# Optimization experiments

Hardware: AMD Instinct MI355X
Metric: run time of the kernel (lower is better)

The kernel has to match this reference:

```python
import jax, jax.numpy as jnp
import numpy as np

N_NODES = 131072
N_EDGES = 262144
N_GRAPHS = 4096
EMB = 300
N_LAYER = 5
N_TASKS = 1
NUM_ATOM_TYPE = 120
NUM_CHIRALITY = 3
NUM_BOND_TYPE = 6   # includes self-loop type 4
NUM_BOND_DIR = 3
SELF_LOOP_TYPE = 4
BN_EPS = 1e-5


def setup_inputs() -> dict:
    key = jax.random.key(0)
    ks = jax.random.split(key, 20)
    x = jnp.stack([
        jax.random.randint(ks[0], (N_NODES,), 0, NUM_ATOM_TYPE, dtype=jnp.int32),
        jax.random.randint(ks[1], (N_NODES,), 0, NUM_CHIRALITY, dtype=jnp.int32),
    ], axis=1)
    edge_index = jax.random.randint(ks[2], (2, N_EDGES), 0, N_NODES, dtype=jnp.int32)
    edge_attr = jnp.stack([
        jax.random.randint(ks[3], (N_EDGES,), 0, 4, dtype=jnp.int32),
        jax.random.randint(ks[4], (N_EDGES,), 0, NUM_BOND_DIR, dtype=jnp.int32),
    ], axis=1)
    # sorted batch vector, every graph non-empty (32 nodes per graph)
    batch = jnp.repeat(jnp.arange(N_GRAPHS, dtype=jnp.int32), N_NODES // N_GRAPHS)
    s = 0.05
    params = {
        'atom_emb0': jax.random.normal(ks[5], (NUM_ATOM_TYPE, EMB), jnp.float32) * s,
        'atom_emb1': jax.random.normal(ks[6], (NUM_CHIRALITY, EMB), jnp.float32) * s,
        'bond_emb0': jax.random.normal(ks[7], (N_LAYER, NUM_BOND_TYPE, EMB), jnp.float32) * s,
        'bond_emb1': jax.random.normal(ks[8], (N_LAYER, NUM_BOND_DIR, EMB), jnp.float32) * s,
        'W1': jax.random.normal(ks[9], (N_LAYER, EMB, 2 * EMB), jnp.float32) * s,
        'b1': jnp.zeros((N_LAYER, 2 * EMB), jnp.float32),
        'W2': jax.random.normal(ks[10], (N_LAYER, 2 * EMB, EMB), jnp.float32) * s,
        'b2': jnp.zeros((N_LAYER, EMB), jnp.float32),
        'bn_gamma': jnp.ones((N_LAYER, EMB), jnp.float32),
        'bn_beta': jnp.zeros((N_LAYER, EMB), jnp.float32),
        'head_W1': jax.random.normal(ks[11], (EMB, EMB // 2), jnp.float32) * s,
        'head_b1': jnp.zeros((EMB // 2,), jnp.float32),
        'head_W2': jax.random.normal(ks[12], (EMB // 2, N_TASKS), jnp.float32) * s,
        'head_b2': jnp.zeros((N_TASKS,), jnp.float32),
    }
    return dict(x=x, edge_index=edge_index, edge_attr=edge_attr, batch=batch,
                num_graphs=N_GRAPHS, **params)


def _gnn_forward(x, edge_index, edge_attr, batch, num_graphs,
                 atom_emb0, atom_emb1, bond_emb0, bond_emb1,
                 W1, b1, W2, b2, bn_gamma, bn_beta,
                 head_W1, head_b1, head_W2, head_b2):
    n = x.shape[0]
    L = W1.shape[0]
    # add self loops with bond type SELF_LOOP_TYPE
    loop = jnp.arange(n, dtype=edge_index.dtype)
    src = jnp.concatenate([edge_index[0], loop])
    dst = jnp.concatenate([edge_index[1], loop])
    ea0 = jnp.concatenate([edge_attr[:, 0], jnp.full((n,), SELF_LOOP_TYPE, edge_attr.dtype)])
    ea1 = jnp.concatenate([edge_attr[:, 1], jnp.zeros((n,), edge_attr.dtype)])

    h = atom_emb0[x[:, 0]] + atom_emb1[x[:, 1]]  # [N, EMB]
    for l in range(L):
        e = bond_emb0[l][ea0] + bond_emb1[l][ea1]           # [E+N, EMB]
        msg = h[src] + e                                     # gather + add
        agg = jax.ops.segment_sum(msg, dst, num_segments=n)  # [N, EMB]
        hid = jax.nn.relu(agg @ W1[l] + b1[l])
        h2 = hid @ W2[l] + b2[l]
        # BatchNorm1d (training-mode batch stats)
        mean = jnp.mean(h2, axis=0)
        var = jnp.var(h2, axis=0)
        h2 = (h2 - mean) * jax.lax.rsqrt(var + BN_EPS) * bn_gamma[l] + bn_beta[l]
        h = h2 if l == L - 1 else jax.nn.relu(h2)
    # super_node_rep: last node of each graph (batch is sorted)
    last_idx = jax.ops.segment_max(jnp.arange(n), batch, num_segments=num_graphs)
    sup = h[last_idx]                                        # [G, EMB]
    out = jax.nn.elu(sup @ head_W1 + head_b1) @ head_W2 + head_b2
    return out                                               # [G, num_tasks]


def reference(x, edge_index, edge_attr, batch, num_graphs,
              atom_emb0, atom_emb1, bond_emb0, bond_emb1,
              W1, b1, W2, b2, bn_gamma, bn_beta,
              head_W1, head_b1, head_W2, head_b2):
    return _gnn_forward(x, edge_index, edge_attr, batch, num_graphs,
                        atom_emb0, atom_emb1, bond_emb0, bond_emb1,
                        W1, b1, W2, b2, bn_gamma, bn_beta,
                        head_W1, head_b1, head_W2, head_b2)
```

## Files before the change

kernel.cpp:

```cpp
#include <hip/hip_runtime.h>
#include <hip/hip_bf16.h>

#define NN 131072
#define NE 262144
#define NG 4096
#define EMB 300
#define HS 320
#define K1 320
#define N1 640
#define N2P 384
#define NLAYER 5
#define NRB (NN / 128)

typedef __attribute__((ext_vector_type(8))) short short8;
typedef __attribute__((ext_vector_type(4))) float f32x4;
typedef __attribute__((ext_vector_type(4))) unsigned short ushort4v;

__device__ __forceinline__ void gload_lds16(const void* g, void* l) {
  __builtin_amdgcn_global_load_lds((const __attribute__((address_space(1))) void*)g,
                                   (__attribute__((address_space(3))) void*)l, 16, 0, 0);
}
__device__ __forceinline__ float b2f(unsigned short u) {
  return __uint_as_float(((unsigned)u) << 16);
}
__device__ __forceinline__ unsigned short f2b(float x) {
  __hip_bfloat16 b = __float2bfloat16(x);
  return *(unsigned short*)&b;
}


__global__ void prep_w1(const float* __restrict__ W1, __hip_bfloat16* __restrict__ W1T) {
  int idx = blockIdx.x * 256 + threadIdx.x;
  if (idx >= NLAYER * N1 * K1) return;
  int l = idx / (N1 * K1); int r = idx % (N1 * K1);
  int n = r / K1; int k = r % K1;
  float v = (n < 600 && k < 300) ? W1[(size_t)(l * 300 + k) * 600 + n] : 0.f;
  W1T[idx] = __float2bfloat16(v);
}

__global__ void prep_w2(const float* __restrict__ W2, __hip_bfloat16* __restrict__ W2T) {
  int idx = blockIdx.x * 256 + threadIdx.x;
  if (idx >= NLAYER * N2P * N1) return;
  int l = idx / (N2P * N1); int r = idx % (N2P * N1);
  int n = r / N1; int k = r % N1;
  float v = (n < 300 && k < 600) ? W2[(size_t)(l * 600 + k) * 300 + n] : 0.f;
  W2T[idx] = __float2bfloat16(v);
}

__global__ void prep_bias(const float* __restrict__ b1, const float* __restrict__ b2,
                          float* __restrict__ b1p, float* __restrict__ b2p) {
  int idx = blockIdx.x * 256 + threadIdx.x;
  if (idx < NLAYER * N1) {
    int l = idx / N1, n = idx % N1;
    b1p[idx] = (n < 600) ? b1[l * 600 + n] : 0.f;
  } else {
    int k = idx - NLAYER * N1;
    if (k < NLAYER * N2P) {
      int l = k / N2P, n = k % N2P;
      b2p[k] = (n < 300) ? b2[l * 300 + n] : 0.f;
    }
  }
}

__global__ void init_h(const int* __restrict__ x, const float* __restrict__ ae0,
                       const float* __restrict__ ae1, __hip_bfloat16* __restrict__ h) {
  int v = blockIdx.x; int t = threadIdx.x;
  int x0 = x[2 * v], x1 = x[2 * v + 1];
  for (int c = t; c < HS; c += 256)
    h[(size_t)v * HS + c] = __float2bfloat16(c < EMB ? ae0[x0 * EMB + c] + ae1[x1 * EMB + c] : 0.f);
}


__global__ void count_edges(const int* __restrict__ ei, int* __restrict__ counts) {
  int j = blockIdx.x * 256 + threadIdx.x;
  if (j >= NE) return;
  atomicAdd(&counts[ei[NE + j]], 1);
}

__global__ void scan_block(const int* __restrict__ counts, int* __restrict__ indptr,
                           int* __restrict__ blockSums) {
  __shared__ int s[256];
  int b = blockIdx.x, t = threadIdx.x;
  int base = b * 1024 + t * 4;
  int4 c = *(const int4*)&counts[base];
  int tsum = c.x + c.y + c.z + c.w;
  s[t] = tsum;
  __syncthreads();
  for (int off = 1; off < 256; off <<= 1) {
    int v = (t >= off) ? s[t - off] : 0;
    __syncthreads();
    s[t] += v;
    __syncthreads();
  }
  int excl = (t == 0) ? 0 : s[t - 1];
  indptr[base + 0] = excl;
  indptr[base + 1] = excl + c.x;
  indptr[base + 2] = excl + c.x + c.y;
  indptr[base + 3] = excl + c.x + c.y + c.z;
  if (t == 255) blockSums[b] = s[255];
}

__global__ void scan_top(const int* __restrict__ blockSums, int* __restrict__ blockOff) {
  __shared__ int s[128];
  int t = threadIdx.x;
  s[t] = blockSums[t];
  __syncthreads();
  for (int off = 1; off < 128; off <<= 1) {
    int v = (t >= off) ? s[t - off] : 0;
    __syncthreads();
    s[t] += v;
    __syncthreads();
  }
  blockOff[t] = (t == 0) ? 0 : s[t - 1];
}

__global__ void scan_add(int* __restrict__ indptr, const int* __restrict__ blockOff) {
  int b = blockIdx.x, t = threadIdx.x;
  int off = blockOff[b];
  int base = b * 1024 + t * 4;
  indptr[base + 0] += off; indptr[base + 1] += off;
  indptr[base + 2] += off; indptr[base + 3] += off;
  if (b == 127 && t == 255) indptr[NN] = NE;
}

__global__ void scatter_edges(const int* __restrict__ ei, const int* __restrict__ ea,
                              int* __restrict__ cursor, int* __restrict__ epacked) {
  int j = blockIdx.x * 256 + threadIdx.x;
  if (j >= NE) return;
  int dst = ei[NE + j];
  int src = ei[j];
  int c = ea[2 * j] * 3 + ea[2 * j + 1];
  int pos = atomicAdd(&cursor[dst], 1);
  epacked[pos] = src | (c << 17);
}

__global__ void last_idx_kernel(const int* __restrict__ batch, int* __restrict__ lastidx) {
  int i = blockIdx.x * 256 + threadIdx.x;
  if (i >= NN) return;
  int b = batch[i];
  if (i == NN - 1 || batch[i + 1] != b) lastidx[b] = i;
}

template<int BN>
__global__ __launch_bounds__(1024)
void aggregate_kernel(const __hip_bfloat16* __restrict__ hg, const int* __restrict__ indptr,
                      const int* __restrict__ epacked,
                      const float* __restrict__ bond0, const float* __restrict__ bond1,
                      const float* __restrict__ bnsc, const float* __restrict__ bnsh,
                      __hip_bfloat16* __restrict__ agg) {
  __shared__ float etab[13 * HS];
  const int tid = threadIdx.x;
  for (int idx = tid; idx < 13 * HS; idx += 1024) {
    int c = idx / HS, ch = idx % HS;
    float val = 0.f;
    if (ch < EMB) {
      int t0 = (c < 12) ? (c / 3) : 4;
      int t1 = (c < 12) ? (c % 3) : 0;
      val = bond0[t0 * EMB + ch] + bond1[t1 * EMB + ch];
    }
    etab[idx] = val;
  }
  __syncthreads();
  const int wid = tid >> 6, lane = tid & 63;
  const int v = blockIdx.x * 16 + wid;
  const int cA = lane * 4, cB = 256 + lane;
  const unsigned short* h = (const unsigned short*)hg;

  f32x4 scA = {1.f, 1.f, 1.f, 1.f}, shA = {0.f, 0.f, 0.f, 0.f};
  float scB = 1.f, shB = 0.f;
  if (BN) {
    scA = *(const f32x4*)&bnsc[cA]; shA = *(const f32x4*)&bnsh[cA];
    scB = bnsc[cB]; shB = bnsh[cB];
  }
  auto trA = [&](float x, int k) -> float {
    if (BN) x = fmaxf(fmaf(x, scA[k], shA[k]), 0.f);
    return x;
  };
  auto trB = [&](float x) -> float {
    if (BN) x = fmaxf(fmaf(x, scB, shB), 0.f);
    return x;
  };

  const unsigned short* hv = h + (size_t)v * HS;
  ushort4v pA = *(const ushort4v*)(hv + cA);
  unsigned short pB = hv[cB];
  const float* es = etab + 12 * HS;
  float a0 = trA(b2f(pA[0]), 0) + es[cA];
  float a1 = trA(b2f(pA[1]), 1) + es[cA + 1];
  float a2 = trA(b2f(pA[2]), 2) + es[cA + 2];
  float a3 = trA(b2f(pA[3]), 3) + es[cA + 3];
  float a4 = trB(b2f(pB)) + es[cB];

  const int jb = indptr[v], je = indptr[v + 1];
  int j = jb;
  for (; j + 2 <= je; j += 2) {
    int p0 = epacked[j], p1 = epacked[j + 1];
    const unsigned short* h0 = h + (size_t)(p0 & (NN - 1)) * HS;
    const unsigned short* h1 = h + (size_t)(p1 & (NN - 1)) * HS;
    ushort4v q0 = *(const ushort4v*)(h0 + cA);
    ushort4v q1 = *(const ushort4v*)(h1 + cA);
    unsigned short r0 = h0[cB], r1 = h1[cB];
    const float* e0 = etab + (p0 >> 17) * HS;
    const float* e1 = etab + (p1 >> 17) * HS;
    a0 += trA(b2f(q0[0]), 0) + e0[cA]     + trA(b2f(q1[0]), 0) + e1[cA];
    a1 += trA(b2f(q0[1]), 1) + e0[cA + 1] + trA(b2f(q1[1]), 1) + e1[cA + 1];
    a2 += trA(b2f(q0[2]), 2) + e0[cA + 2] + trA(b2f(q1[2]), 2) + e1[cA + 2];
    a3 += trA(b2f(q0[3]), 3) + e0[cA + 3] + trA(b2f(q1[3]), 3) + e1[cA + 3];
    a4 += trB(b2f(r0)) + e0[cB] + trB(b2f(r1)) + e1[cB];
  }
  if (j < je) {
    int p0 = epacked[j];
    const unsigned short* h0 = h + (size_t)(p0 & (NN - 1)) * HS;
    ushort4v q0 = *(const ushort4v*)(h0 + cA);
    unsigned short r0 = h0[cB];
    const float* e0 = etab + (p0 >> 17) * HS;
    a0 += trA(b2f(q0[0]), 0) + e0[cA];
    a1 += trA(b2f(q0[1]), 1) + e0[cA + 1];
    a2 += trA(b2f(q0[2]), 2) + e0[cA + 2];
    a3 += trA(b2f(q0[3]), 3) + e0[cA + 3];
    a4 += trB(b2f(r0)) + e0[cB];
  }

  unsigned short* av = (unsigned short*)agg + (size_t)v * HS;
  ushort4v o; o[0] = f2b(a0); o[1] = f2b(a1); o[2] = f2b(a2); o[3] = f2b(a3);
  *(ushort4v*)(av + cA) = o;
  av[cB] = f2b(a4);
}

template<int RELU, int STATS, int NBN>
__global__ __launch_bounds__(256)
void gemm_kernel(const short* __restrict__ A, const short* __restrict__ BT,
                 const float* __restrict__ bias, __hip_bfloat16* __restrict__ Cout,
                 float* __restrict__ part, int K, int outStride, int outBound, int rbBase) {
  __shared__ short smem[2 * 8192];
  __shared__ float sred[STATS ? 128 : 1][2];
  const int tid = threadIdx.x;
  const int wid = tid >> 6, lane = tid & 63;
  const int wm = wid >> 1, wn = wid & 1;
  f32x4 acc[4][4] = {};

  const int cpx = gridDim.x >> 3;
  const int logical = (blockIdx.x & 7) * cpx + (blockIdx.x >> 3);
  const int bn = logical % NBN;
  const int bm = logical / NBN;

  const short* Ag = A + (size_t)bm * 128 * K;
  const short* Bg = BT + (size_t)bn * 128 * K;
  const int r2 = tid >> 2;
  const int ksw = ((tid & 3) ^ ((tid >> 3) & 3)) * 8;
  const int arow_h = lane & 15;
  const int koffR = (((lane >> 4) ^ ((arow_h >> 1) & 3)) * 8);

  auto stage = [&](int buf, int kt) {
    short* s = smem + buf * 8192;
    const short* Ao = Ag + (size_t)r2 * K + kt + ksw;
    const short* Bo = Bg + (size_t)r2 * K + kt + ksw;
    gload_lds16(Ao,          s + tid * 8);
    gload_lds16(Ao + 64 * K, s + 2048 + tid * 8);
    gload_lds16(Bo,          s + 4096 + tid * 8);
    gload_lds16(Bo + 64 * K, s + 6144 + tid * 8);
  };

  const int NT = K >> 5;
  stage(0, 0);
  for (int t = 0; t < NT; ++t) {
    if (t + 1 < NT) {
      stage((t + 1) & 1, (t + 1) * 32);
      asm volatile("s_waitcnt vmcnt(4)" ::: "memory");
    } else {
      asm volatile("s_waitcnt vmcnt(0)" ::: "memory");
    }
    __builtin_amdgcn_s_barrier();
    const short* sA = smem + (t & 1) * 8192 + wm * 2048;
    const short* sB = smem + (t & 1) * 8192 + 4096 + wn * 2048;
    short8 af[4], bf[4];
#pragma unroll
    for (int i = 0; i < 4; i++) af[i] = *(const short8*)&sA[(arow_h + i * 16) * 32 + koffR];
#pragma unroll
    for (int j = 0; j < 4; j++) bf[j] = *(const short8*)&sB[(arow_h + j * 16) * 32 + koffR];
#pragma unroll
    for (int i = 0; i < 4; i++)
#pragma unroll
      for (int j = 0; j < 4; j++)
        acc[i][j] = __builtin_amdgcn_mfma_f32_16x16x32_bf16(af[i], bf[j], acc[i][j], 0, 0, 0);
    asm volatile("s_waitcnt lgkmcnt(0)" ::: "memory");
    __builtin_amdgcn_s_barrier();
  }

  const int row0 = bm * 128 + wm * 64 + (lane >> 4) * 4;
  const int col0 = bn * 128 + wn * 64 + (lane & 15);
  float bs[4];
#pragma unroll
  for (int j = 0; j < 4; j++) bs[j] = bias[col0 + j * 16];
  float ssum[4] = {0, 0, 0, 0}, ssq[4] = {0, 0, 0, 0};
  if (STATS) {
    if (tid < 128) { sred[tid][0] = 0.f; sred[tid][1] = 0.f; }
    __syncthreads();
  }
#pragma unroll
  for (int i = 0; i < 4; i++) {
#pragma unroll
    for (int p = 0; p < 4; p++) {
      const size_t row = row0 + i * 16 + p;
#pragma unroll
      for (int j = 0; j < 4; j++) {
        const int col = col0 + j * 16;
        float v = acc[i][j][p] + bs[j];
        if (STATS) { ssum[j] += v; ssq[j] += v * v; }
        if (RELU) v = fmaxf(v, 0.f);
        if (col < outBound)
          Cout[row * (size_t)outStride + col] = __float2bfloat16(v);
      }
    }
  }
  if (STATS) {
#pragma unroll
    for (int j = 0; j < 4; j++) {
      const int cw = wn * 64 + j * 16 + (lane & 15);
      atomicAdd(&sred[cw][0], ssum[j]);
      atomicAdd(&sred[cw][1], ssq[j]);
    }
    __syncthreads();
    if (tid < 128) {
      const int col = bn * 128 + tid;
      if (col < EMB) {
        const int rb = rbBase + bm;
        part[(size_t)col * (2 * NRB) + rb] = sred[tid][0];
        part[(size_t)col * (2 * NRB) + NRB + rb] = sred[tid][1];
      }
    }
  }
}

__global__ __launch_bounds__(256)
void bn_finalize(const float* __restrict__ part, const float* __restrict__ gamma,
                 const float* __restrict__ beta, float* __restrict__ bnsc,
                 float* __restrict__ bnsh) {
  __shared__ float rs[256], rq[256];
  const int c = blockIdx.x, t = threadIdx.x;
  if (c >= EMB) {
    if (t == 0) { bnsc[c] = 0.f; bnsh[c] = 0.f; }
    return;
  }
  float s = 0.f, q = 0.f;
  for (int rb = t; rb < NRB; rb += 256) {
    s += part[(size_t)c * (2 * NRB) + rb];
    q += part[(size_t)c * (2 * NRB) + NRB + rb];
  }
  rs[t] = s; rq[t] = q;
  __syncthreads();
  for (int off = 128; off > 0; off >>= 1) {
    if (t < off) { rs[t] += rs[t + off]; rq[t] += rq[t + off]; }
    __syncthreads();
  }
  if (t == 0) {
    float mean = rs[0] / (float)NN;
    float var = rq[0] / (float)NN - mean * mean;
    float sc = rsqrtf(var + 1e-5f) * gamma[c];
    bnsc[c] = sc;
    bnsh[c] = beta[c] - mean * sc;
  }
}

__global__ __launch_bounds__(256)
void head_kernel(const __hip_bfloat16* __restrict__ h, const int* __restrict__ lastidx,
                 const float* __restrict__ bnsc4, const float* __restrict__ bnsh4,
                 const float* __restrict__ hW1, const float* __restrict__ hb1,
                 const float* __restrict__ hW2, const float* __restrict__ hb2,
                 float* __restrict__ out) {
  __shared__ float sup[EMB];
  __shared__ float red[256];
  int g = blockIdx.x, t = threadIdx.x;
  int v = lastidx[g];
  for (int c = t; c < EMB; c += 256)
    sup[c] = b2f(((const unsigned short*)h)[(size_t)v * HS + c]) * bnsc4[c] + bnsh4[c];
  __syncthreads();
  float val = 0.f;
  if (t < 150) {
    float acc = hb1[t];
    for (int k = 0; k < EMB; k++) acc += sup[k] * hW1[k * 150 + t];
    float e = (acc > 0.f) ? acc : (expf(acc) - 1.f);
    val = e * hW2[t];
  }
  red[t] = val;
  __syncthreads();
  for (int off = 128; off > 0; off >>= 1) {
    if (t < off) red[t] += red[t + off];
    __syncthreads();
  }
  if (t == 0) out[g] = red[0] + hb2[0];
}


extern "C" void kernel_launch(void* const* d_in, const int* in_sizes, int n_in,
                              void* d_out, int out_size, void* d_ws, size_t ws_size,
                              hipStream_t stream) {
  const int* x      = (const int*)d_in[0];
  const int* ei     = (const int*)d_in[1];
  const int* ea     = (const int*)d_in[2];
  const int* batch  = (const int*)d_in[3];
  const float* atom0 = (const float*)d_in[5];
  const float* atom1 = (const float*)d_in[6];
  const float* bond0 = (const float*)d_in[7];
  const float* bond1 = (const float*)d_in[8];
  const float* W1    = (const float*)d_in[9];
  const float* b1    = (const float*)d_in[10];
  const float* W2    = (const float*)d_in[11];
  const float* b2    = (const float*)d_in[12];
  const float* gamma = (const float*)d_in[13];
  const float* beta  = (const float*)d_in[14];
  const float* hW1   = (const float*)d_in[15];
  const float* hb1   = (const float*)d_in[16];
  const float* hW2   = (const float*)d_in[17];
  const float* hb2   = (const float*)d_in[18];
  float* out = (float*)d_out;

  char* p = (char*)d_ws;
  auto carve = [&](size_t b) -> void* {
    void* r = (void*)p;
    p += (b + 255) & ~(size_t)255;
    return r;
  };
  __hip_bfloat16* agg = (__hip_bfloat16*)carve((size_t)NN * HS * 2);
  __hip_bfloat16* h   = (__hip_bfloat16*)carve((size_t)NN * HS * 2);
  __hip_bfloat16* W1T = (__hip_bfloat16*)carve((size_t)NLAYER * N1 * K1 * 2);
  __hip_bfloat16* W2T = (__hip_bfloat16*)carve((size_t)NLAYER * N2P * N1 * 2);
  float* b1p          = (float*)carve((size_t)NLAYER * N1 * 4);
  float* b2p          = (float*)carve((size_t)NLAYER * N2P * 4);
  float* part         = (float*)carve((size_t)EMB * 2 * NRB * 4);
  float* bnsc         = (float*)carve((size_t)NLAYER * HS * 4);
  float* bnsh         = (float*)carve((size_t)NLAYER * HS * 4);
  int* counts         = (int*)carve((size_t)NN * 4);
  int* indptr         = (int*)carve((size_t)(NN + 1) * 4);
  int* cursor         = (int*)carve((size_t)NN * 4);
  int* epacked        = (int*)carve((size_t)NE * 4);
  int* blockSums      = (int*)carve(128 * 4);
  int* blockOff       = (int*)carve(128 * 4);
  int* lastidx        = (int*)carve((size_t)NG * 4);

  size_t used = (size_t)(p - (char*)d_ws);
  size_t avail = (ws_size > used + 4096) ? (ws_size - used - 4096) : 0;
  int CHUNK = 16384;
  if (avail >= (size_t)65536 * N1 * 2) CHUNK = 65536;
  else if (avail >= (size_t)32768 * N1 * 2) CHUNK = 32768;
  __hip_bfloat16* hid = (__hip_bfloat16*)carve((size_t)CHUNK * N1 * 2);

  hipMemsetAsync(counts, 0, (size_t)NN * 4, stream);

  prep_w1<<<(NLAYER * N1 * K1 + 255) / 256, 256, 0, stream>>>(W1, W1T);
  prep_w2<<<(NLAYER * N2P * N1 + 255) / 256, 256, 0, stream>>>(W2, W2T);
  prep_bias<<<(NLAYER * (N1 + N2P) + 255) / 256, 256, 0, stream>>>(b1, b2, b1p, b2p);
  init_h<<<NN, 256, 0, stream>>>(x, atom0, atom1, h);

  count_edges<<<NE / 256, 256, 0, stream>>>(ei, counts);
  scan_block<<<128, 256, 0, stream>>>(counts, indptr, blockSums);
  scan_top<<<1, 128, 0, stream>>>(blockSums, blockOff);
  scan_add<<<128, 256, 0, stream>>>(indptr, blockOff);
  hipMemcpyAsync(cursor, indptr, (size_t)NN * 4, hipMemcpyDeviceToDevice, stream);
  scatter_edges<<<NE / 256, 256, 0, stream>>>(ei, ea, cursor, epacked);
  last_idx_kernel<<<NN / 256, 256, 0, stream>>>(batch, lastidx);

  for (int l = 0; l < NLAYER; l++) {
    if (l == 0)
      aggregate_kernel<0><<<NN / 16, 1024, 0, stream>>>(
          h, indptr, epacked, bond0 + (size_t)l * 6 * EMB, bond1 + (size_t)l * 3 * EMB,
          nullptr, nullptr, agg);
    else
      aggregate_kernel<1><<<NN / 16, 1024, 0, stream>>>(
          h, indptr, epacked, bond0 + (size_t)l * 6 * EMB, bond1 + (size_t)l * 3 * EMB,
          bnsc + (size_t)(l - 1) * HS, bnsh + (size_t)(l - 1) * HS, agg);
    for (int c0 = 0; c0 < NN; c0 += CHUNK) {
      gemm_kernel<1, 0, N1 / 128><<<(CHUNK / 128) * (N1 / 128), 256, 0, stream>>>(
          (const short*)(agg + (size_t)c0 * HS),
          (const short*)(W1T + (size_t)l * N1 * K1), b1p + l * N1,
          hid, nullptr, K1, N1, N1, 0);
      gemm_kernel<0, 1, N2P / 128><<<(CHUNK / 128) * (N2P / 128), 256, 0, stream>>>(
          (const short*)hid,
          (const short*)(W2T + (size_t)l * N2P * N1), b2p + l * N2P,
          h + (size_t)c0 * HS, part, N1, HS, HS, c0 / 128);
    }
    bn_finalize<<<HS, 256, 0, stream>>>(part, gamma + (size_t)l * EMB, beta + (size_t)l * EMB,
                                        bnsc + (size_t)l * HS, bnsh + (size_t)l * HS);
  }

  head_kernel<<<NG, 256, 0, stream>>>(h, lastidx, bnsc + 4 * HS, bnsh + 4 * HS,
                                      hW1, hb1, hW2, hb2, out);
}
```

Baseline: 1.862 ms.

## Precompute bond tables, process more nodes per aggregate block, skip padded GEMM columns

The per-layer bond embedding table is now built once by a prep kernel instead of inside every aggregate block, and each aggregate block handles 64 nodes instead of 16, so the table-fill cost is spread over four times as many nodes. In the second GEMM, the last column tile (columns 256-383, of which only up to 300 are real) skips loading the upper B half and idles the wave covering columns 320-383, which hold only padding. This cuts redundant table construction and wasted MFMA work. In exchange there are four times fewer aggregate blocks, which may reduce latency hiding, and the GEMM gets some wave divergence.

```diff
diff --git a/kernel.cpp b/kernel.cpp
--- a/kernel.cpp
+++ b/kernel.cpp
@@ -62,6 +62,21 @@
   }
 }
 
+__global__ void prep_etab(const float* __restrict__ bond0, const float* __restrict__ bond1,
+                          float* __restrict__ etabg) {
+  int idx = blockIdx.x * 256 + threadIdx.x;
+  if (idx >= NLAYER * 13 * HS) return;
+  int l = idx / (13 * HS); int r = idx % (13 * HS);
+  int c = r / HS; int ch = r % HS;
+  float val = 0.f;
+  if (ch < EMB) {
+    int t0 = (c < 12) ? (c / 3) : 4;
+    int t1 = (c < 12) ? (c % 3) : 0;
+    val = bond0[(size_t)(l * 6 + t0) * EMB + ch] + bond1[(size_t)(l * 3 + t1) * EMB + ch];
+  }
+  etabg[idx] = val;
+}
+
 __global__ void init_h(const int* __restrict__ x, const float* __restrict__ ae0,
                        const float* __restrict__ ae1, __hip_bfloat16* __restrict__ h) {
   int v = blockIdx.x; int t = threadIdx.x;
@@ -144,25 +159,16 @@
 template<int BN>
 __global__ __launch_bounds__(1024)
 void aggregate_kernel(const __hip_bfloat16* __restrict__ hg, const int* __restrict__ indptr,
-                      const int* __restrict__ epacked,
-                      const float* __restrict__ bond0, const float* __restrict__ bond1,
+                      const int* __restrict__ epacked, const float* __restrict__ etabg,
                       const float* __restrict__ bnsc, const float* __restrict__ bnsh,
                       __hip_bfloat16* __restrict__ agg) {
   __shared__ float etab[13 * HS];
   const int tid = threadIdx.x;
-  for (int idx = tid; idx < 13 * HS; idx += 1024) {
-    int c = idx / HS, ch = idx % HS;
-    float val = 0.f;
-    if (ch < EMB) {
-      int t0 = (c < 12) ? (c / 3) : 4;
-      int t1 = (c < 12) ? (c % 3) : 0;
-      val = bond0[t0 * EMB + ch] + bond1[t1 * EMB + ch];
-    }
-    etab[idx] = val;
-  }
+#pragma unroll
+  for (int idx = tid; idx < 13 * HS; idx += 1024)
+    etab[idx] = etabg[idx];
   __syncthreads();
   const int wid = tid >> 6, lane = tid & 63;
-  const int v = blockIdx.x * 16 + wid;
   const int cA = lane * 4, cB = 256 + lane;
   const unsigned short* h = (const unsigned short*)hg;
 
@@ -180,51 +186,54 @@
     if (BN) x = fmaxf(fmaf(x, scB, shB), 0.f);
     return x;
   };
-
-  const unsigned short* hv = h + (size_t)v * HS;
-  ushort4v pA = *(const ushort4v*)(hv + cA);
-  unsigned short pB = hv[cB];
   const float* es = etab + 12 * HS;
-  float a0 = trA(b2f(pA[0]), 0) + es[cA];
-  float a1 = trA(b2f(pA[1]), 1) + es[cA + 1];
-  float a2 = trA(b2f(pA[2]), 2) + es[cA + 2];
-  float a3 = trA(b2f(pA[3]), 3) + es[cA + 3];
-  float a4 = trB(b2f(pB)) + es[cB];
-
-  const int jb = indptr[v], je = indptr[v + 1];
-  int j = jb;
-  for (; j + 2 <= je; j += 2) {
-    int p0 = epacked[j], p1 = epacked[j + 1];
-    const unsigned short* h0 = h + (size_t)(p0 & (NN - 1)) * HS;
-    const unsigned short* h1 = h + (size_t)(p1 & (NN - 1)) * HS;
-    ushort4v q0 = *(const ushort4v*)(h0 + cA);
-    ushort4v q1 = *(const ushort4v*)(h1 + cA);
-    unsigned short r0 = h0[cB], r1 = h1[cB];
-    const float* e0 = etab + (p0 >> 17) * HS;
-    const float* e1 = etab + (p1 >> 17) * HS;
-    a0 += trA(b2f(q0[0]), 0) + e0[cA]     + trA(b2f(q1[0]), 0) + e1[cA];
-    a1 += trA(b2f(q0[1]), 1) + e0[cA + 1] + trA(b2f(q1[1]), 1) + e1[cA + 1];
-    a2 += trA(b2f(q0[2]), 2) + e0[cA + 2] + trA(b2f(q1[2]), 2) + e1[cA + 2];
-    a3 += trA(b2f(q0[3]), 3) + e0[cA + 3] + trA(b2f(q1[3]), 3) + e1[cA + 3];
-    a4 += trB(b2f(r0)) + e0[cB] + trB(b2f(r1)) + e1[cB];
-  }
-  if (j < je) {
-    int p0 = epacked[j];
-    const unsigned short* h0 = h + (size_t)(p0 & (NN - 1)) * HS;
-    ushort4v q0 = *(const ushort4v*)(h0 + cA);
-    unsigned short r0 = h0[cB];
-    const float* e0 = etab + (p0 >> 17) * HS;
-    a0 += trA(b2f(q0[0]), 0) + e0[cA];
-    a1 += trA(b2f(q0[1]), 1) + e0[cA + 1];
-    a2 += trA(b2f(q0[2]), 2) + e0[cA + 2];
-    a3 += trA(b2f(q0[3]), 3) + e0[cA + 3];
-    a4 += trB(b2f(r0)) + e0[cB];
-  }
-
-  unsigned short* av = (unsigned short*)agg + (size_t)v * HS;
-  ushort4v o; o[0] = f2b(a0); o[1] = f2b(a1); o[2] = f2b(a2); o[3] = f2b(a3);
-  *(ushort4v*)(av + cA) = o;
-  av[cB] = f2b(a4);
+
+  for (int it = 0; it < 4; ++it) {
+    const int v = blockIdx.x * 64 + it * 16 + wid;
+    const unsigned short* hv = h + (size_t)v * HS;
+    ushort4v pA = *(const ushort4v*)(hv + cA);
+    unsigned short pB = hv[cB];
+    float a0 = trA(b2f(pA[0]), 0) + es[cA];
+    float a1 = trA(b2f(pA[1]), 1) + es[cA + 1];
+    float a2 = trA(b2f(pA[2]), 2) + es[cA + 2];
+    float a3 = trA(b2f(pA[3]), 3) + es[cA + 3];
+    float a4 = trB(b2f(pB)) + es[cB];
+
+    const int jb = indptr[v], je = indptr[v + 1];
+    int j = jb;
+    for (; j + 2 <= je; j += 2) {
+      int p0 = epacked[j], p1 = epacked[j + 1];
+      const unsigned short* h0 = h + (size_t)(p0 & (NN - 1)) * HS;
+      const unsigned short* h1 = h + (size_t)(p1 & (NN - 1)) * HS;
+      ushort4v q0 = *(const ushort4v*)(h0 + cA);
+      ushort4v q1 = *(const ushort4v*)(h1 + cA);
+      unsigned short r0 = h0[cB], r1 = h1[cB];
+      const float* e0 = etab + (p0 >> 17) * HS;
+      const float* e1 = etab + (p1 >> 17) * HS;
+      a0 += trA(b2f(q0[0]), 0) + e0[cA]     + trA(b2f(q1[0]), 0) + e1[cA];
+      a1 += trA(b2f(q0[1]), 1) + e0[cA + 1] + trA(b2f(q1[1]), 1) + e1[cA + 1];
+      a2 += trA(b2f(q0[2]), 2) + e0[cA + 2] + trA(b2f(q1[2]), 2) + e1[cA + 2];
+      a3 += trA(b2f(q0[3]), 3) + e0[cA + 3] + trA(b2f(q1[3]), 3) + e1[cA + 3];
+      a4 += trB(b2f(r0)) + e0[cB] + trB(b2f(r1)) + e1[cB];
+    }
+    if (j < je) {
+      int p0 = epacked[j];
+      const unsigned short* h0 = h + (size_t)(p0 & (NN - 1)) * HS;
+      ushort4v q0 = *(const ushort4v*)(h0 + cA);
+      unsigned short r0 = h0[cB];
+      const float* e0 = etab + (p0 >> 17) * HS;
+      a0 += trA(b2f(q0[0]), 0) + e0[cA];
+      a1 += trA(b2f(q0[1]), 1) + e0[cA + 1];
+      a2 += trA(b2f(q0[2]), 2) + e0[cA + 2];
+      a3 += trA(b2f(q0[3]), 3) + e0[cA + 3];
+      a4 += trB(b2f(r0)) + e0[cB];
+    }
+
+    unsigned short* av = (unsigned short*)agg + (size_t)v * HS;
+    ushort4v o; o[0] = f2b(a0); o[1] = f2b(a1); o[2] = f2b(a2); o[3] = f2b(a3);
+    *(ushort4v*)(av + cA) = o;
+    av[cB] = f2b(a4);
+  }
 }
 
 template<int RELU, int STATS, int NBN>
@@ -244,6 +253,9 @@
   const int bn = logical % NBN;
   const int bm = logical / NBN;
 
+  const bool narrow = (NBN == 3) && (bn == NBN - 1);
+  const bool deadWave = narrow && (wn == 1);
+
   const short* Ag = A + (size_t)bm * 128 * K;
   const short* Bg = BT + (size_t)bn * 128 * K;
   const int r2 = tid >> 2;
@@ -258,7 +270,7 @@
     gload_lds16(Ao,          s + tid * 8);
     gload_lds16(Ao + 64 * K, s + 2048 + tid * 8);
     gload_lds16(Bo,          s + 4096 + tid * 8);
-    gload_lds16(Bo + 64 * K, s + 6144 + tid * 8);
+    if (!narrow) gload_lds16(Bo + 64 * K, s + 6144 + tid * 8);
   };
 
   const int NT = K >> 5;
@@ -266,59 +278,66 @@
   for (int t = 0; t < NT; ++t) {
     if (t + 1 < NT) {
       stage((t + 1) & 1, (t + 1) * 32);
-      asm volatile("s_waitcnt vmcnt(4)" ::: "memory");
+      if (narrow) asm volatile("s_waitcnt vmcnt(3)" ::: "memory");
+      else        asm volatile("s_waitcnt vmcnt(4)" ::: "memory");
     } else {
       asm volatile("s_waitcnt vmcnt(0)" ::: "memory");
     }
     __builtin_amdgcn_s_barrier();
-    const short* sA = smem + (t & 1) * 8192 + wm * 2048;
-    const short* sB = smem + (t & 1) * 8192 + 4096 + wn * 2048;
-    short8 af[4], bf[4];
-#pragma unroll
-    for (int i = 0; i < 4; i++) af[i] = *(const short8*)&sA[(arow_h + i * 16) * 32 + koffR];
-#pragma unroll
-    for (int j = 0; j < 4; j++) bf[j] = *(const short8*)&sB[(arow_h + j * 16) * 32 + koffR];
-#pragma unroll
-    for (int i = 0; i < 4; i++)
-#pragma unroll
-      for (int j = 0; j < 4; j++)
-        acc[i][j] = __builtin_amdgcn_mfma_f32_16x16x32_bf16(af[i], bf[j], acc[i][j], 0, 0, 0);
+    if (!deadWave) {
+      const short* sA = smem + (t & 1) * 8192 + wm * 2048;
+      const short* sB = smem + (t & 1) * 8192 + 4096 + wn * 2048;
+      short8 af[4], bf[4];
+#pragma unroll
+      for (int i = 0; i < 4; i++) af[i] = *(const short8*)&sA[(arow_h + i * 16) * 32 + koffR];
+#pragma unroll
+      for (int j = 0; j < 4; j++) bf[j] = *(const short8*)&sB[(arow_h + j * 16) * 32 + koffR];
+#pragma unroll
+      for (int i = 0; i < 4; i++)
+#pragma unroll
+        for (int j = 0; j < 4; j++)
+          acc[i][j] = __builtin_amdgcn_mfma_f32_16x16x32_bf16(af[i], bf[j], acc[i][j], 0, 0, 0);
+    }
     asm volatile("s_waitcnt lgkmcnt(0)" ::: "memory");
     __builtin_amdgcn_s_barrier();
   }
 
   const int row0 = bm * 128 + wm * 64 + (lane >> 4) * 4;
   const int col0 = bn * 128 + wn * 64 + (lane & 15);
-  float bs[4];
-#pragma unroll
-  for (int j = 0; j < 4; j++) bs[j] = bias[col0 + j * 16];
   float ssum[4] = {0, 0, 0, 0}, ssq[4] = {0, 0, 0, 0};
   if (STATS) {
     if (tid < 128) { sred[tid][0] = 0.f; sred[tid][1] = 0.f; }
     __syncthreads();
   }
-#pragma unroll
-  for (int i = 0; i < 4; i++) {
-#pragma unroll
-    for (int p = 0; p < 4; p++) {
-      const size_t row = row0 + i * 16 + p;
+  if (!deadWave) {
+    float bs[4];
+#pragma unroll
+    for (int j = 0; j < 4; j++) bs[j] = bias[col0 + j * 16];
+#pragma unroll
+    for (int i = 0; i < 4; i++) {
+#pragma unroll
+      for (int p = 0; p < 4; p++) {
+        const size_t row = row0 + i * 16 + p;
+#pragma unroll
+        for (int j = 0; j < 4; j++) {
+          const int col = col0 + j * 16;
+          float v = acc[i][j][p] + bs[j];
+          if (STATS) { ssum[j] += v; ssq[j] += v * v; }
+          if (RELU) v = fmaxf(v, 0.f);
+          if (col < outBound)
+            Cout[row * (size_t)outStride + col] = __float2bfloat16(v);
+        }
+      }
+    }
+  }
+  if (STATS) {
+    if (!deadWave) {
 #pragma unroll
       for (int j = 0; j < 4; j++) {
-        const int col = col0 + j * 16;
-        float v = acc[i][j][p] + bs[j];
-        if (STATS) { ssum[j] += v; ssq[j] += v * v; }
-        if (RELU) v = fmaxf(v, 0.f);
-        if (col < outBound)
-          Cout[row * (size_t)outStride + col] = __float2bfloat16(v);
+        const int cw = wn * 64 + j * 16 + (lane & 15);
+        atomicAdd(&sred[cw][0], ssum[j]);
+        atomicAdd(&sred[cw][1], ssq[j]);
       }
-    }
-  }
-  if (STATS) {
-#pragma unroll
-    for (int j = 0; j < 4; j++) {
-      const int cw = wn * 64 + j * 16 + (lane & 15);
-      atomicAdd(&sred[cw][0], ssum[j]);
-      atomicAdd(&sred[cw][1], ssq[j]);
     }
     __syncthreads();
     if (tid < 128) {
@@ -427,6 +446,7 @@
   __hip_bfloat16* W2T = (__hip_bfloat16*)carve((size_t)NLAYER * N2P * N1 * 2);
   float* b1p          = (float*)carve((size_t)NLAYER * N1 * 4);
   float* b2p          = (float*)carve((size_t)NLAYER * N2P * 4);
+  float* etabg        = (float*)carve((size_t)NLAYER * 13 * HS * 4);
   float* part         = (float*)carve((size_t)EMB * 2 * NRB * 4);
   float* bnsc         = (float*)carve((size_t)NLAYER * HS * 4);
   float* bnsh         = (float*)carve((size_t)NLAYER * HS * 4);
@@ -450,6 +470,7 @@
   prep_w1<<<(NLAYER * N1 * K1 + 255) / 256, 256, 0, stream>>>(W1, W1T);
   prep_w2<<<(NLAYER * N2P * N1 + 255) / 256, 256, 0, stream>>>(W2, W2T);
   prep_bias<<<(NLAYER * (N1 + N2P) + 255) / 256, 256, 0, stream>>>(b1, b2, b1p, b2p);
+  prep_etab<<<(NLAYER * 13 * HS + 255) / 256, 256, 0, stream>>>(bond0, bond1, etabg);
   init_h<<<NN, 256, 0, stream>>>(x, atom0, atom1, h);
 
   count_edges<<<NE / 256, 256, 0, stream>>>(ei, counts);
@@ -462,12 +483,11 @@
 
   for (int l = 0; l < NLAYER; l++) {
     if (l == 0)
-      aggregate_kernel<0><<<NN / 16, 1024, 0, stream>>>(
-          h, indptr, epacked, bond0 + (size_t)l * 6 * EMB, bond1 + (size_t)l * 3 * EMB,
-          nullptr, nullptr, agg);
+      aggregate_kernel<0><<<NN / 64, 1024, 0, stream>>>(
+          h, indptr, epacked, etabg + (size_t)l * 13 * HS, nullptr, nullptr, agg);
     else
-      aggregate_kernel<1><<<NN / 16, 1024, 0, stream>>>(
-          h, indptr, epacked, bond0 + (size_t)l * 6 * EMB, bond1 + (size_t)l * 3 * EMB,
+      aggregate_kernel<1><<<NN / 64, 1024, 0, stream>>>(
+          h, indptr, epacked, etabg + (size_t)l * 13 * HS,
           bnsc + (size_t)(l - 1) * HS, bnsh + (size_t)(l - 1) * HS, agg);
     for (int c0 = 0; c0 < NN; c0 += CHUNK) {
       gemm_kernel<1, 0, N1 / 128><<<(CHUNK / 128) * (N1 / 128), 256, 0, stream>>>(
```

Result: slower. 1.907 ms (+2.4%).
